# Performance work log

Hardware: AMD Instinct MI355X
Metric: run time of the kernel (lower is better)

## Reference

```python
import jax, jax.numpy as jnp
import numpy as np


def setup_inputs() -> dict:
    key = jax.random.key(0)
    k_x, k_q, k_k, k_v = jax.random.split(key, 4)
    seq_len, d_in, d_out = 4096, 1024, 1024
    x = jax.random.normal(k_x, (seq_len, d_in), dtype=jnp.float32)
    # torch nn.Linear weights are [d_out, d_in]; applied as x @ W.T
    scale = 1.0 / np.sqrt(d_in)
    Wq = jax.random.uniform(k_q, (d_out, d_in), jnp.float32, -scale, scale)
    Wk = jax.random.uniform(k_k, (d_out, d_in), jnp.float32, -scale, scale)
    Wv = jax.random.uniform(k_v, (d_out, d_in), jnp.float32, -scale, scale)
    return {"x": x, "Wq": Wq, "Wk": Wk, "Wv": Wv}


def reference(x, Wq, Wk, Wv):
    # x: [S, d_in]; Wq/Wk/Wv: [d_out, d_in]
    queries = x @ Wq.T          # [S, d_out]
    keys = x @ Wk.T             # [S, d_out]
    values = x @ Wv.T           # [S, d_out]
    d_k = keys.shape[-1]
    attn_scores = queries @ keys.T                      # [S, S]
    attn_weights = jax.nn.softmax(attn_scores / jnp.sqrt(jnp.float32(d_k)), axis=-1)
    S = attn_scores.shape[0]
    tril = jnp.tril(jnp.ones((S, S), dtype=attn_weights.dtype))
    masked = tril * attn_weights
    masked_norm = masked / jnp.sum(masked, axis=-1, keepdims=True)
    context_vec = masked_norm @ values                  # [S, d_out]
    return context_vec
```

## Files before the change

kernel.cpp:

```cpp
#include <hip/hip_runtime.h>
#include <hip/hip_bf16.h>


typedef __bf16 bf16_t;
typedef __bf16 bf16x4v __attribute__((ext_vector_type(4)));
typedef __bf16 bf16x8 __attribute__((ext_vector_type(8)));
typedef float f32x4 __attribute__((ext_vector_type(4)));
typedef unsigned char u8;
typedef long long i64_t;

#define AS1 __attribute__((address_space(1)))
#define AS3 __attribute__((address_space(3)))

__device__ __forceinline__ void async_copy16(const void* g, void* l) {
    __builtin_amdgcn_global_load_lds((AS1 void*)(g), (AS3 void*)(l), 16, 0, 0);
}

__device__ __forceinline__ u8 f32_to_fp8(float v) {
    return (u8)(__builtin_amdgcn_cvt_pk_fp8_f32(v, v, 0, false) & 0xff);
}

__device__ __forceinline__ void store_conv(float* p, float v) { *p = v; }
__device__ __forceinline__ void store_conv(bf16_t* p, float v) { *p = (bf16_t)v; }
__device__ __forceinline__ void store_conv(u8* p, float v) { *p = f32_to_fp8(v); }

template <int EPI, typename OutT>
__device__ __forceinline__ void gemm_tile_bf16(const bf16_t* __restrict__ A, int lda,
                                               const bf16_t* __restrict__ B, int ldb,
                                               OutT* __restrict__ C, int ldc,
                                               int kb0, int kb1, float alpha,
                                               bf16_t* __restrict__ As,
                                               bf16_t* __restrict__ Bs,
                                               const float* __restrict__ inv) {
    constexpr int BK = 64;
    const int tid = threadIdx.x;
    const int lane = tid & 63, wave = tid >> 6;
    const int wm = wave >> 1, wn = wave & 1;
    const int q = lane >> 4, l16 = lane & 15;

    f32x4 acc[4][4] = {};

    const bf16_t* aSrc[4];
    const bf16_t* bSrc[4];
    int ldsOff[4];
#pragma unroll
    for (int it = 0; it < 4; ++it) {
        int c = it * 256 + tid;
        int r = c >> 3, b = c & 7;
        int sb = b ^ (r & 7);
        aSrc[it] = A + (size_t)r * lda + sb * 8;
        bSrc[it] = B + (size_t)r * ldb + sb * 8;
        ldsOff[it] = c * 8;
    }

    for (int kb = kb0; kb < kb1; ++kb) {
        const int k0 = kb * BK;
#pragma unroll
        for (int it = 0; it < 4; ++it) async_copy16(aSrc[it] + k0, &As[ldsOff[it]]);
#pragma unroll
        for (int it = 0; it < 4; ++it) async_copy16(bSrc[it] + k0, &Bs[ldsOff[it]]);
        __syncthreads();

#pragma unroll
        for (int k2 = 0; k2 < 2; ++k2) {
            bf16x8 af[4], bfr[4];
#pragma unroll
            for (int mt = 0; mt < 4; ++mt) {
                int m = wm * 64 + mt * 16 + l16;
                int blk = (k2 * 4 + q) ^ (m & 7);
                af[mt] = *(const bf16x8*)&As[m * BK + blk * 8];
            }
#pragma unroll
            for (int nt = 0; nt < 4; ++nt) {
                int nn = wn * 64 + nt * 16 + l16;
                int blk = (k2 * 4 + q) ^ (nn & 7);
                bfr[nt] = *(const bf16x8*)&Bs[nn * BK + blk * 8];
            }
#pragma unroll
            for (int mt = 0; mt < 4; ++mt)
#pragma unroll
                for (int nt = 0; nt < 4; ++nt)
                    acc[mt][nt] = __builtin_amdgcn_mfma_f32_16x16x32_bf16(
                        af[mt], bfr[nt], acc[mt][nt], 0, 0, 0);
        }
        __syncthreads();
    }

    const int row0 = wm * 64, col0 = wn * 64;
#pragma unroll
    for (int mt = 0; mt < 4; ++mt)
#pragma unroll
        for (int nt = 0; nt < 4; ++nt)
#pragma unroll
            for (int r = 0; r < 4; ++r) {
                int lr = row0 + mt * 16 + q * 4 + r;
                float v = acc[mt][nt][r];
                v = (EPI == 2) ? v * inv[lr] : v * alpha;
                store_conv(&C[(size_t)lr * ldc + col0 + nt * 16 + l16], v);
            }
}

__device__ __forceinline__ void scores_tile_fp8(const u8* __restrict__ A, int lda,
                                                const u8* __restrict__ B, int ldb,
                                                bf16_t* __restrict__ C, int ldc,
                                                float alpha,
                                                u8* __restrict__ As, u8* __restrict__ Bs,
                                                float* __restrict__ partial,
                                                int gr0, int gc0,
                                                float* __restrict__ sred) {
    const int tid = threadIdx.x;
    const int lane = tid & 63, wave = tid >> 6;
    const int wm = wave >> 1, wn = wave & 1;
    const int q = lane >> 4, l16 = lane & 15;

    f32x4 acc[4][2] = {};

    const u8* aSrc[4];
    int aOff[4];
#pragma unroll
    for (int it = 0; it < 4; ++it) {
        int c = it * 256 + tid;
        int r = c >> 3, b = c & 7;
        int sb = b ^ (r & 7);
        aSrc[it] = A + (size_t)r * lda + sb * 16;
        aOff[it] = c * 16;
    }
    const u8* bSrc[2];
    int bOff[2];
#pragma unroll
    for (int it = 0; it < 2; ++it) {
        int c = it * 256 + tid;
        int r = c >> 3, b = c & 7;
        int sb = b ^ (r & 7);
        bSrc[it] = B + (size_t)r * ldb + sb * 16;
        bOff[it] = c * 16;
    }

    for (int kb = 0; kb < 8; ++kb) {
        const int k0 = kb * 128;
#pragma unroll
        for (int it = 0; it < 4; ++it) async_copy16(aSrc[it] + k0, &As[aOff[it]]);
#pragma unroll
        for (int it = 0; it < 2; ++it) async_copy16(bSrc[it] + k0, &Bs[bOff[it]]);
        __syncthreads();

#pragma unroll
        for (int k2 = 0; k2 < 4; ++k2) {
            i64_t af[4], bfr[2];
            const int cb = 2 * k2 + (q >> 1), co = (q & 1) * 8;
#pragma unroll
            for (int mt = 0; mt < 4; ++mt) {
                int m = wm * 64 + mt * 16 + l16;
                af[mt] = *(const i64_t*)&As[m * 128 + ((cb ^ (m & 7)) << 4) + co];
            }
#pragma unroll
            for (int nt = 0; nt < 2; ++nt) {
                int nn = wn * 32 + nt * 16 + l16;
                bfr[nt] = *(const i64_t*)&Bs[nn * 128 + ((cb ^ (nn & 7)) << 4) + co];
            }
#pragma unroll
            for (int mt = 0; mt < 4; ++mt)
#pragma unroll
                for (int nt = 0; nt < 2; ++nt)
                    acc[mt][nt] = __builtin_amdgcn_mfma_f32_16x16x32_fp8_fp8(
                        af[mt], bfr[nt], acc[mt][nt], 0, 0, 0);
        }
        __syncthreads();
    }

    const int row0 = wm * 64, col0 = wn * 32;
    float esum[4][4];
#pragma unroll
    for (int mt = 0; mt < 4; ++mt)
#pragma unroll
        for (int r = 0; r < 4; ++r) esum[mt][r] = 0.f;
#pragma unroll
    for (int mt = 0; mt < 4; ++mt)
#pragma unroll
        for (int nt = 0; nt < 2; ++nt)
#pragma unroll
            for (int r = 0; r < 4; ++r) {
                int lr = row0 + mt * 16 + q * 4 + r;
                int lc = col0 + nt * 16 + l16;
                float p = (gc0 + lc > gr0 + lr) ? 0.f : __expf(acc[mt][nt][r] * alpha);
                esum[mt][r] += p;
                C[(size_t)lr * ldc + lc] = (bf16_t)p;
            }
#pragma unroll
    for (int mt = 0; mt < 4; ++mt)
#pragma unroll
        for (int r = 0; r < 4; ++r) {
#pragma unroll
            for (int off = 1; off < 16; off <<= 1)
                esum[mt][r] += __shfl_xor(esum[mt][r], off, 64);
            if (l16 == 0) sred[(row0 + mt * 16 + q * 4 + r) * 2 + wn] = esum[mt][r];
        }
    __syncthreads();
    if (tid < 128) partial[(size_t)tid * 64] = sred[tid * 2] + sred[tid * 2 + 1];
}

__global__ __launch_bounds__(256) void k_qkv(const bf16_t* __restrict__ xb,
                                             const bf16_t* __restrict__ wqk,
                                             const bf16_t* __restrict__ wvb,
                                             u8* __restrict__ qk,
                                             bf16_t* __restrict__ vt) {
    __shared__ __attribute__((aligned(16))) bf16_t As[128 * 64];
    __shared__ __attribute__((aligned(16))) bf16_t Bs[128 * 64];
    int b = blockIdx.x;
    if (b < 512) {
        int bm = b & 31, bn = b >> 5;
        gemm_tile_bf16<0, u8>(xb + (size_t)bm * 128 * 1024, 1024,
                              wqk + (size_t)bn * 128 * 1024, 1024,
                              qk + (size_t)bm * 128 * 2048 + bn * 128, 2048,
                              0, 16, 1.f, As, Bs, nullptr);
    } else {
        int t = b - 512;
        int bm = t & 7, bn = t >> 3;
        gemm_tile_bf16<0, bf16_t>(wvb + (size_t)bm * 128 * 1024, 1024,
                                  xb + (size_t)bn * 128 * 1024, 1024,
                                  vt + (size_t)bm * 128 * 4096 + bn * 128, 4096,
                                  0, 16, 1.f, As, Bs, nullptr);
    }
}

__global__ __launch_bounds__(256) void k_scores(const u8* __restrict__ qk,
                                                bf16_t* __restrict__ P,
                                                float* __restrict__ rowsum_part) {
    __shared__ __attribute__((aligned(16))) u8 As[128 * 128];
    __shared__ __attribute__((aligned(16))) u8 Bs[64 * 128];
    __shared__ float sred[128 * 2];
    int t = blockIdx.x;
    int bm = (int)((sqrtf(4.f * (float)t + 1.f) - 1.f) * 0.5f);
    while (bm * bm + bm > t) --bm;
    while ((bm + 1) * (bm + 1) + (bm + 1) <= t) ++bm;
    int bn = t - bm * bm - bm;
    scores_tile_fp8(qk + (size_t)bm * 128 * 2048, 2048,
                    qk + 1024 + (size_t)bn * 64 * 2048, 2048,
                    P + (size_t)bm * 128 * 4096 + bn * 64, 4096,
                    0.03125f, As, Bs,
                    rowsum_part + (size_t)bm * 128 * 64 + bn,
                    bm * 128, bn * 64, sred);
}

__global__ __launch_bounds__(256) void k_rowsum(const float* __restrict__ rowsum_part,
                                                float* __restrict__ inv_sum) {
    int i = threadIdx.x * 16 + blockIdx.x;
    int nt = (i >> 6) + 1;
    float s = 0.f;
    for (int u = 0; u < nt; ++u) s += rowsum_part[(size_t)i * 64 + u];
    inv_sum[i] = 1.f / s;
}

__global__ __launch_bounds__(256) void k_pv(const bf16_t* __restrict__ P,
                                            const bf16_t* __restrict__ vt,
                                            const float* __restrict__ inv_sum,
                                            float* __restrict__ out,
                                            float* __restrict__ partials) {
    __shared__ __attribute__((aligned(16))) bf16_t As[128 * 64];
    __shared__ __attribute__((aligned(16))) bf16_t Bs[128 * 64];
    int b = blockIdx.x;
    int bn = b & 7, g = b >> 3;
    int bm, s;
    if (g < 6)       { bm = g;                 s = 0; }
    else if (g < 18) { bm = 6 + (g - 6) / 2;   s = (g - 6) % 2; }
    else if (g < 36) { bm = 12 + (g - 18) / 3; s = (g - 18) % 3; }
    else if (g < 60) { bm = 18 + (g - 36) / 4; s = (g - 36) % 4; }
    else if (g < 90) { bm = 24 + (g - 60) / 5; s = (g - 60) % 5; }
    else             { bm = 30 + (g - 90) / 6; s = (g - 90) % 6; }
    int nk = 2 * (bm + 1);
    int ns = (nk + 11) / 12;
    int kb0 = s * nk / ns;
    int kb1 = (s + 1) * nk / ns;

    const bf16_t* A = P + (size_t)bm * 128 * 4096;
    const bf16_t* B = vt + (size_t)bn * 128 * 4096;
    if (ns == 1) {
        gemm_tile_bf16<2, float>(A, 4096, B, 4096,
                                 out + (size_t)bm * 128 * 1024 + bn * 128, 1024,
                                 kb0, kb1, 1.f, As, Bs, inv_sum + bm * 128);
    } else {
        int cum = (bm < 12) ? (bm - 6) * 2
                : (bm < 18) ? 12 + (bm - 12) * 3
                : (bm < 24) ? 30 + (bm - 18) * 4
                : (bm < 30) ? 54 + (bm - 24) * 5
                            : 84 + (bm - 30) * 6;
        gemm_tile_bf16<0, float>(A, 4096, B, 4096,
                                 partials + ((size_t)(cum + s) * 8 + bn) * 16384, 128,
                                 kb0, kb1, 1.f, As, Bs, nullptr);
    }
}

__global__ __launch_bounds__(256) void k_reduce(const float* __restrict__ partials,
                                                const float* __restrict__ inv_sum,
                                                float* __restrict__ out) {
    int b = blockIdx.x;
    int t = b % 208, p = b / 208;
    int bm = t % 26 + 6, bn = t / 26;
    int ns = (2 * (bm + 1) + 11) / 12;
    int cum = (bm < 12) ? (bm - 6) * 2
            : (bm < 18) ? 12 + (bm - 12) * 3
            : (bm < 24) ? 30 + (bm - 18) * 4
            : (bm < 30) ? 54 + (bm - 24) * 5
                        : 84 + (bm - 30) * 6;
    int idx = p * 1024 + threadIdx.x * 4;
    int lr = idx >> 7, lc = idx & 127;
    float sx = 0.f, sy = 0.f, sz = 0.f, sw = 0.f;
    for (int u = 0; u < ns; ++u) {
        const float4 v = *(const float4*)(partials + ((size_t)(cum + u) * 8 + bn) * 16384 + idx);
        sx += v.x; sy += v.y; sz += v.z; sw += v.w;
    }
    float inv = inv_sum[bm * 128 + lr];
    float4 o = {sx * inv, sy * inv, sz * inv, sw * inv};
    *(float4*)(out + (size_t)(bm * 128 + lr) * 1024 + bn * 128 + lc) = o;
}

__global__ __launch_bounds__(256) void cast_to_bf16(const float* __restrict__ x,
                                                    const float* __restrict__ Wq,
                                                    const float* __restrict__ Wk,
                                                    const float* __restrict__ Wv,
                                                    bf16_t* __restrict__ xb,
                                                    bf16_t* __restrict__ wqk,
                                                    bf16_t* __restrict__ wv) {
    const int NX = (4096 * 1024) / 4;
    const int NW = (1024 * 1024) / 4;
    int idx = blockIdx.x * 256 + threadIdx.x;
    const float* src;
    bf16_t* dst;
    int off;
    if (idx < NX) {
        src = x; dst = xb; off = idx;
    } else if (idx < NX + NW) {
        src = Wq; dst = wqk; off = idx - NX;
    } else if (idx < NX + 2 * NW) {
        src = Wk; dst = wqk + (size_t)NW * 4; off = idx - NX - NW;
    } else {
        src = Wv; dst = wv; off = idx - NX - 2 * NW;
    }
    float4 f = ((const float4*)src)[off];
    bf16x4v o;
    o.x = (bf16_t)f.x; o.y = (bf16_t)f.y; o.z = (bf16_t)f.z; o.w = (bf16_t)f.w;
    *(bf16x4v*)(dst + (size_t)off * 4) = o;
}

extern "C" void kernel_launch(void* const* d_in, const int* in_sizes, int n_in,
                              void* d_out, int out_size, void* d_ws, size_t ws_size,
                              hipStream_t stream) {
    (void)in_sizes; (void)n_in; (void)out_size; (void)ws_size;
    const float* x  = (const float*)d_in[0];
    const float* Wq = (const float*)d_in[1];
    const float* Wk = (const float*)d_in[2];
    const float* Wv = (const float*)d_in[3];
    float* out = (float*)d_out;

    char* ws = (char*)d_ws;
    bf16_t* xb   = (bf16_t*)(ws + (size_t)0);
    bf16_t* wqk  = (bf16_t*)(ws + ((size_t)8 << 20));
    bf16_t* wvb  = (bf16_t*)(ws + ((size_t)12 << 20));
    u8*     qk   = (u8*)(ws + ((size_t)14 << 20));
    bf16_t* vt   = (bf16_t*)(ws + ((size_t)22 << 20));
    bf16_t* P    = (bf16_t*)(ws + ((size_t)30 << 20));
    float* rowsp = (float*)(ws + ((size_t)62 << 20));
    float* invs  = (float*)(ws + ((size_t)63 << 20));
    float* parts = (float*)(ws + ((size_t)64 << 20));

    cast_to_bf16<<<7168, 256, 0, stream>>>(x, Wq, Wk, Wv, xb, wqk, wvb);

    k_qkv<<<768, 256, 0, stream>>>(xb, wqk, wvb, qk, vt);

    k_scores<<<1056, 256, 0, stream>>>(qk, P, rowsp);

    k_rowsum<<<16, 256, 0, stream>>>(rowsp, invs);

    k_pv<<<816, 256, 0, stream>>>(P, vt, invs, out, parts);
    k_reduce<<<3328, 256, 0, stream>>>(parts, invs, out);
}
```

Before: 200.5 us.

## Fuse row-sum reduction into PV/reduce and rebalance split-K schedule

Removes the separate rowsum kernel. The last scores tile in each row zeroes the unused partial-sum slots, and the PV and reduce kernels then compute inverse row sums on the fly from the 64 partials. The split-K partitioning of the causal PV GEMM changes to at most 4 splits over quarter bands, which reduces block count and reduce traffic. The QKV GEMM block order is also swizzled into groups of 4 M-tiles for better L2 reuse of weight tiles. In exchange, the row-sum work is repeated in many blocks, and the coarser split may leave the largest tiles imbalanced.

Measured after the change: 198.2 us. No clear change (-1.2%).

```diff
diff --git a/kernel.cpp b/kernel.cpp
--- a/kernel.cpp
+++ b/kernel.cpp
@@ -23,6 +23,17 @@
 __device__ __forceinline__ void store_conv(float* p, float v) { *p = v; }
 __device__ __forceinline__ void store_conv(bf16_t* p, float v) { *p = (bf16_t)v; }
 __device__ __forceinline__ void store_conv(u8* p, float v) { *p = f32_to_fp8(v); }
+
+__device__ __forceinline__ float sum64(const float* p) {
+    const f32x4* v = (const f32x4*)p;
+    float s = 0.f;
+#pragma unroll
+    for (int u = 0; u < 16; ++u) {
+        f32x4 a = v[u];
+        s += a[0] + a[1] + a[2] + a[3];
+    }
+    return s;
+}
 
 template <int EPI, typename OutT>
 __device__ __forceinline__ void gemm_tile_bf16(const bf16_t* __restrict__ A, int lda,
@@ -208,7 +219,8 @@
     __shared__ __attribute__((aligned(16))) bf16_t Bs[128 * 64];
     int b = blockIdx.x;
     if (b < 512) {
-        int bm = b & 31, bn = b >> 5;
+        int bmi = b & 3, bn = (b >> 2) & 15, bmo = b >> 6;
+        int bm = bmo * 4 + bmi;
         gemm_tile_bf16<0, u8>(xb + (size_t)bm * 128 * 1024, 1024,
                               wqk + (size_t)bn * 128 * 1024, 1024,
                               qk + (size_t)bm * 128 * 2048 + bn * 128, 2048,
@@ -240,50 +252,47 @@
                     0.03125f, As, Bs,
                     rowsum_part + (size_t)bm * 128 * 64 + bn,
                     bm * 128, bn * 64, sred);
-}
-
-__global__ __launch_bounds__(256) void k_rowsum(const float* __restrict__ rowsum_part,
-                                                float* __restrict__ inv_sum) {
-    int i = threadIdx.x * 16 + blockIdx.x;
-    int nt = (i >> 6) + 1;
-    float s = 0.f;
-    for (int u = 0; u < nt; ++u) s += rowsum_part[(size_t)i * 64 + u];
-    inv_sum[i] = 1.f / s;
+    if (bn == 2 * bm + 1) {
+        float* rp = rowsum_part + (size_t)bm * 128 * 64;
+        int tid = threadIdx.x;
+        for (int r = tid >> 4; r < 128; r += 16)
+            for (int u = 2 * bm + 2 + (tid & 15); u < 64; u += 16)
+                rp[r * 64 + u] = 0.f;
+    }
 }
 
 __global__ __launch_bounds__(256) void k_pv(const bf16_t* __restrict__ P,
                                             const bf16_t* __restrict__ vt,
-                                            const float* __restrict__ inv_sum,
+                                            const float* __restrict__ rowsum_part,
                                             float* __restrict__ out,
                                             float* __restrict__ partials) {
     __shared__ __attribute__((aligned(16))) bf16_t As[128 * 64];
     __shared__ __attribute__((aligned(16))) bf16_t Bs[128 * 64];
+    __shared__ float sInv[128];
     int b = blockIdx.x;
     int bn = b & 7, g = b >> 3;
-    int bm, s;
-    if (g < 6)       { bm = g;                 s = 0; }
-    else if (g < 18) { bm = 6 + (g - 6) / 2;   s = (g - 6) % 2; }
-    else if (g < 36) { bm = 12 + (g - 18) / 3; s = (g - 18) % 3; }
-    else if (g < 60) { bm = 18 + (g - 36) / 4; s = (g - 36) % 4; }
-    else if (g < 90) { bm = 24 + (g - 60) / 5; s = (g - 60) % 5; }
-    else             { bm = 30 + (g - 90) / 6; s = (g - 90) % 6; }
+    int bm, s, ns;
+    if (g < 8)       { bm = g;                 s = 0;            ns = 1; }
+    else if (g < 24) { bm = 8 + (g - 8) / 2;   s = (g - 8) % 2;  ns = 2; }
+    else if (g < 48) { bm = 16 + (g - 24) / 3; s = (g - 24) % 3; ns = 3; }
+    else             { bm = 24 + (g - 48) / 4; s = (g - 48) % 4; ns = 4; }
     int nk = 2 * (bm + 1);
-    int ns = (nk + 11) / 12;
     int kb0 = s * nk / ns;
     int kb1 = (s + 1) * nk / ns;
 
     const bf16_t* A = P + (size_t)bm * 128 * 4096;
     const bf16_t* B = vt + (size_t)bn * 128 * 4096;
     if (ns == 1) {
+        int tid = threadIdx.x;
+        if (tid < 128)
+            sInv[tid] = 1.f / sum64(rowsum_part + (size_t)(bm * 128 + tid) * 64);
         gemm_tile_bf16<2, float>(A, 4096, B, 4096,
                                  out + (size_t)bm * 128 * 1024 + bn * 128, 1024,
-                                 kb0, kb1, 1.f, As, Bs, inv_sum + bm * 128);
+                                 kb0, kb1, 1.f, As, Bs, sInv);
     } else {
-        int cum = (bm < 12) ? (bm - 6) * 2
-                : (bm < 18) ? 12 + (bm - 12) * 3
-                : (bm < 24) ? 30 + (bm - 18) * 4
-                : (bm < 30) ? 54 + (bm - 24) * 5
-                            : 84 + (bm - 30) * 6;
+        int cum = (bm < 16) ? (bm - 8) * 2
+                : (bm < 24) ? 16 + (bm - 16) * 3
+                            : 40 + (bm - 24) * 4;
         gemm_tile_bf16<0, float>(A, 4096, B, 4096,
                                  partials + ((size_t)(cum + s) * 8 + bn) * 16384, 128,
                                  kb0, kb1, 1.f, As, Bs, nullptr);
@@ -291,25 +300,31 @@
 }
 
 __global__ __launch_bounds__(256) void k_reduce(const float* __restrict__ partials,
-                                                const float* __restrict__ inv_sum,
+                                                const float* __restrict__ rowsum_part,
                                                 float* __restrict__ out) {
     int b = blockIdx.x;
-    int t = b % 208, p = b / 208;
-    int bm = t % 26 + 6, bn = t / 26;
-    int ns = (2 * (bm + 1) + 11) / 12;
-    int cum = (bm < 12) ? (bm - 6) * 2
-            : (bm < 18) ? 12 + (bm - 12) * 3
-            : (bm < 24) ? 30 + (bm - 18) * 4
-            : (bm < 30) ? 54 + (bm - 24) * 5
-                        : 84 + (bm - 30) * 6;
-    int idx = p * 1024 + threadIdx.x * 4;
+    int t = b % 192, p = b / 192;
+    int bm = t % 24 + 8, bn = t / 24;
+    int ns = (bm < 16) ? 2 : (bm < 24) ? 3 : 4;
+    int cum = (bm < 16) ? (bm - 8) * 2
+            : (bm < 24) ? 16 + (bm - 16) * 3
+                        : 40 + (bm - 24) * 4;
+    __shared__ float sInv[8];
+    int tid = threadIdx.x;
+    if (tid < 8) {
+        int row = bm * 128 + p * 8 + tid;
+        sInv[tid] = 1.f / sum64(rowsum_part + (size_t)row * 64);
+    }
+    __syncthreads();
+
+    int idx = p * 1024 + tid * 4;
     int lr = idx >> 7, lc = idx & 127;
     float sx = 0.f, sy = 0.f, sz = 0.f, sw = 0.f;
     for (int u = 0; u < ns; ++u) {
         const float4 v = *(const float4*)(partials + ((size_t)(cum + u) * 8 + bn) * 16384 + idx);
         sx += v.x; sy += v.y; sz += v.z; sw += v.w;
     }
-    float inv = inv_sum[bm * 128 + lr];
+    float inv = sInv[lr - p * 8];
     float4 o = {sx * inv, sy * inv, sz * inv, sw * inv};
     *(float4*)(out + (size_t)(bm * 128 + lr) * 1024 + bn * 128 + lc) = o;
 }
@@ -360,7 +375,6 @@
     bf16_t* vt   = (bf16_t*)(ws + ((size_t)22 << 20));
     bf16_t* P    = (bf16_t*)(ws + ((size_t)30 << 20));
     float* rowsp = (float*)(ws + ((size_t)62 << 20));
-    float* invs  = (float*)(ws + ((size_t)63 << 20));
     float* parts = (float*)(ws + ((size_t)64 << 20));
 
     cast_to_bf16<<<7168, 256, 0, stream>>>(x, Wq, Wk, Wv, xb, wqk, wvb);
@@ -369,8 +383,6 @@
 
     k_scores<<<1056, 256, 0, stream>>>(qk, P, rowsp);
 
-    k_rowsum<<<16, 256, 0, stream>>>(rowsp, invs);
-
-    k_pv<<<816, 256, 0, stream>>>(P, vt, invs, out, parts);
-    k_reduce<<<3328, 256, 0, stream>>>(parts, invs, out);
-}
+    k_pv<<<640, 256, 0, stream>>>(P, vt, rowsp, out, parts);
+    k_reduce<<<3072, 256, 0, stream>>>(parts, rowsp, out);
+}
```
